# Kernel tuning notes

Measured on AMD Instinct MI355X. Metric: run time of the kernel, lower is better.

## Reference

```python
import jax, jax.numpy as jnp
import numpy as np

N = 50000
D = 128
E = 600000
ALPHA = 0.1
THETA = 0.5
LAYER = 1


def setup_inputs() -> dict:
    key = jax.random.key(0)
    k1, k2, k3, k4, k5, k6 = jax.random.split(key, 6)
    x = jax.random.normal(k1, (N, D), dtype=jnp.float32)
    x0 = jax.random.normal(k2, (N, D), dtype=jnp.float32)
    edge_index = jax.random.randint(k3, (2, E), 0, N, dtype=jnp.int64)
    norm = jax.random.uniform(k4, (E,), dtype=jnp.float32)
    # Linear weight, torch nn.Linear default init: U(-1/sqrt(fan_in), 1/sqrt(fan_in))
    bound = 1.0 / np.sqrt(D)
    W = jax.random.uniform(k5, (D, D), dtype=jnp.float32, minval=-bound, maxval=bound)
    return {"x": x, "x0": x0, "edge_index": edge_index, "norm": norm, "W": W}


def reference(x, x0, edge_index, norm, W):
    row, col = edge_index[0], edge_index[1]
    # gather source features, scale per-edge, scatter-add into destinations
    msgs = x[row] * norm[:, None]                      # [E, D]
    h = jax.ops.segment_sum(msgs, col, num_segments=N)  # [N, D]
    h = (1.0 - ALPHA) * h + ALPHA * x0
    beta = np.log(THETA / LAYER + 1.0).astype(np.float32)
    # lin(h) = h @ W.T (torch Linear applies x @ W^T)
    h = (1.0 - beta) * h + beta * (h @ W.T)
    return h
```

## Files before the change

### kernel.cpp

```cpp
#include <hip/hip_runtime.h>

#define DIM 128
#define ALPHA 0.1f
#define BETA 0.40546510810816438f

typedef __attribute__((ext_vector_type(8))) short short8v;
typedef __attribute__((ext_vector_type(4))) float float4v;

static __device__ inline unsigned short f2bf(float f) {
  union { float f; unsigned u; } a;
  a.f = f;
  unsigned r = a.u + 0x7fff + ((a.u >> 16) & 1);
  return (unsigned short)(r >> 16);
}

__global__ __launch_bounds__(256) void prep(const int* __restrict__ col,
                                            int* __restrict__ counts,
                                            int* __restrict__ rank,
                                            const float* __restrict__ x,
                                            short* __restrict__ xb,
                                            const float* __restrict__ W,
                                            short* __restrict__ Wb,
                                            int E, int total4, int cntBlocks,
                                            int cvtXBlocks) {
  int b = blockIdx.x;
  if (b < cntBlocks) {
    int e = b * 256 + threadIdx.x;
    if (e < E) rank[e] = atomicAdd(&counts[col[e]], 1);
  } else if (b < cntBlocks + cvtXBlocks) {
    int i = (b - cntBlocks) * 256 + threadIdx.x;
    if (i < total4) {
      float4 v = ((const float4*)x)[i];
      ((short4*)xb)[i] = make_short4((short)f2bf(v.x), (short)f2bf(v.y),
                                     (short)f2bf(v.z), (short)f2bf(v.w));
    }
  } else {
    int i = (b - cntBlocks - cvtXBlocks) * 256 + threadIdx.x;
    if (i < 128 * 32) {
      float4 v = ((const float4*)W)[i];
      ((short4*)Wb)[i] = make_short4((short)f2bf(v.x), (short)f2bf(v.y),
                                     (short)f2bf(v.z), (short)f2bf(v.w));
    }
  }
}

__global__ __launch_bounds__(256) void scan_blocks(const int* __restrict__ counts,
                                                   int* __restrict__ offsets,
                                                   int* __restrict__ blockSums, int N) {
  __shared__ int sm[256];
  int tid = threadIdx.x;
  int gid = blockIdx.x * 256 + tid;
  int v = (gid < N) ? counts[gid] : 0;
  sm[tid] = v;
  __syncthreads();
  for (int off = 1; off < 256; off <<= 1) {
    int t = (tid >= off) ? sm[tid - off] : 0;
    __syncthreads();
    sm[tid] += t;
    __syncthreads();
  }
  if (gid < N) offsets[gid] = sm[tid] - v;
  if (tid == 255) blockSums[blockIdx.x] = sm[255];
}

__global__ __launch_bounds__(256) void scan_off(int* __restrict__ offsets,
                                                const int* __restrict__ blockSums,
                                                int N, int E, int nb) {
  __shared__ int sm[256];
  int tid = threadIdx.x;
  int v = (tid < nb) ? blockSums[tid] : 0;
  sm[tid] = v;
  __syncthreads();
  for (int off = 1; off < 256; off <<= 1) {
    int t = (tid >= off) ? sm[tid - off] : 0;
    __syncthreads();
    sm[tid] += t;
    __syncthreads();
  }
  int excl = sm[tid] - v;
  __syncthreads();
  sm[tid] = excl;
  __syncthreads();
  int pref = sm[blockIdx.x];

  int gid = blockIdx.x * 256 + tid;
  if (gid < N) offsets[gid] += pref;
  else if (gid == N) offsets[N] = E;
}

__global__ __launch_bounds__(256) void fill_edges(const int* __restrict__ row,
                                                  const int* __restrict__ col,
                                                  const float* __restrict__ nrm,
                                                  const int* __restrict__ offsets,
                                                  const int* __restrict__ rank,
                                                  int2* __restrict__ emeta, int E) {
  int e = blockIdx.x * 256 + threadIdx.x;
  if (e >= E) return;
  int c = col[e];
  int idx = offsets[c] + rank[e];
  float s = (1.0f - ALPHA) * nrm[e];
  emeta[idx] = make_int2(row[e], __float_as_int(s));
}

__global__ __launch_bounds__(256) void gather_gemm(const unsigned* __restrict__ xb,
                                                   const float* __restrict__ x0,
                                                   const int* __restrict__ offs,
                                                   const int2* __restrict__ emeta,
                                                   const short* __restrict__ Wb,
                                                   float* __restrict__ out, int N) {
  __shared__ unsigned short hb[16][136];
  const int tid = threadIdx.x;
  const int lane = tid & 63;
  const int wave = tid >> 6;
  const int row0 = blockIdx.x * 16;

  for (int q = 0; q < 4; ++q) {
    const int lr = wave * 4 + q;
    const int n = row0 + lr;
    unsigned packed = 0;
    if (n < N) {
      int s = offs[n], t = offs[n + 1];
      float accx[8], accy[8];
#pragma unroll
      for (int j = 0; j < 8; ++j) { accx[j] = 0.0f; accy[j] = 0.0f; }
      for (int base = s; base < t; base += 64) {
        int r = 0;
        float sc = 0.0f;
        if (base + lane < t) {
          int2 m = emeta[base + lane];
          r = m.x;
          sc = __int_as_float(m.y);
        }
        int cnt = t - base;
        if (cnt > 64) cnt = 64;
        int cnt8 = (cnt + 7) & ~7;
        for (int i = 0; i < cnt8; i += 8) {
#pragma unroll
          for (int j = 0; j < 8; ++j) {
            int rj = __shfl(r, i + j);
            float sj = __shfl(sc, i + j);
            unsigned u = xb[(size_t)rj * (DIM / 2) + lane];
            accx[j] += sj * __uint_as_float(u << 16);
            accy[j] += sj * __uint_as_float(u & 0xffff0000u);
          }
        }
      }
      float sx = ((accx[0] + accx[1]) + (accx[2] + accx[3])) +
                 ((accx[4] + accx[5]) + (accx[6] + accx[7]));
      float sy = ((accy[0] + accy[1]) + (accy[2] + accy[3])) +
                 ((accy[4] + accy[5]) + (accy[6] + accy[7]));
      float2 v0 = *(const float2*)(x0 + (size_t)n * DIM + 2 * lane);
      float hx = sx + ALPHA * v0.x;
      float hy = sy + ALPHA * v0.y;
      packed = (unsigned)f2bf(hx) | ((unsigned)f2bf(hy) << 16);
    }
    *(unsigned*)&hb[lr][2 * lane] = packed;
  }
  __syncthreads();

  const int arow = lane & 15;
  const int kg = (lane >> 4) * 8;
  short8v a[4];
#pragma unroll
  for (int s = 0; s < 4; ++s) a[s] = *(const short8v*)&hb[arow][s * 32 + kg];

#pragma unroll
  for (int j2 = 0; j2 < 2; ++j2) {
    const int jt = wave * 2 + j2;
    const int bcol = jt * 16 + (lane & 15);
    float4v acc = {0.0f, 0.0f, 0.0f, 0.0f};
#pragma unroll
    for (int s = 0; s < 4; ++s) {
      short8v b = *(const short8v*)(Wb + (size_t)bcol * DIM + s * 32 + kg);
      acc = __builtin_amdgcn_mfma_f32_16x16x32_bf16(a[s], b, acc, 0, 0, 0);
    }
    const int lr0 = (lane >> 4) << 2;
#pragma unroll
    for (int p = 0; p < 4; ++p) {
      int R = row0 + lr0 + p;
      if (R < N) {
        int c = jt * 16 + (lane & 15);
        float hv = __uint_as_float(((unsigned)hb[lr0 + p][c]) << 16);
        out[(size_t)R * DIM + c] = (1.0f - BETA) * hv + BETA * acc[p];
      }
    }
  }
}

__global__ __launch_bounds__(256) void count_edges(const int* __restrict__ col,
                                                   int* __restrict__ counts,
                                                   int* __restrict__ rank, int E) {
  int e = blockIdx.x * 256 + threadIdx.x;
  if (e < E) rank[e] = atomicAdd(&counts[col[e]], 1);
}

__global__ __launch_bounds__(256) void gather_nodes_f32(const float* __restrict__ x,
                                                        const float* __restrict__ x0,
                                                        const int* __restrict__ offs,
                                                        const int2* __restrict__ emeta,
                                                        float* __restrict__ h, int N) {
  int lane = threadIdx.x & 63;
  int gwave = blockIdx.x * 4 + (threadIdx.x >> 6);
  int nwaves = gridDim.x * 4;
  int dbase = 2 * lane;
  for (int n = gwave; n < N; n += nwaves) {
    int s = offs[n], t = offs[n + 1];
    float ax = 0, ay = 0, bx = 0, by = 0;
    for (int base = s; base < t; base += 64) {
      int r = 0;
      float sc = 0.0f;
      if (base + lane < t) {
        int2 m = emeta[base + lane];
        r = m.x;
        sc = __int_as_float(m.y);
      }
      int cnt = t - base;
      if (cnt > 64) cnt = 64;
      int cnt4 = (cnt + 3) & ~3;
      for (int i = 0; i < cnt4; i += 4) {
        int r0 = __shfl(r, i), r1 = __shfl(r, i + 1);
        int r2 = __shfl(r, i + 2), r3 = __shfl(r, i + 3);
        float s0 = __shfl(sc, i), s1 = __shfl(sc, i + 1);
        float s2 = __shfl(sc, i + 2), s3 = __shfl(sc, i + 3);
        float2 v0 = *(const float2*)(x + (size_t)r0 * DIM + dbase);
        float2 v1 = *(const float2*)(x + (size_t)r1 * DIM + dbase);
        float2 v2 = *(const float2*)(x + (size_t)r2 * DIM + dbase);
        float2 v3 = *(const float2*)(x + (size_t)r3 * DIM + dbase);
        ax += s0 * v0.x; ay += s0 * v0.y;
        bx += s1 * v1.x; by += s1 * v1.y;
        ax += s2 * v2.x; ay += s2 * v2.y;
        bx += s3 * v3.x; by += s3 * v3.y;
      }
    }
    float2 v0 = *(const float2*)(x0 + (size_t)n * DIM + dbase);
    float2 hv;
    hv.x = (ax + bx) + ALPHA * v0.x;
    hv.y = (ay + by) + ALPHA * v0.y;
    *(float2*)(h + (size_t)n * DIM + dbase) = hv;
  }
}

__global__ __launch_bounds__(256) void final_mfma(const float* __restrict__ W,
                                                  float* __restrict__ out, int N) {
  __shared__ short W_s[128][136];
  __shared__ short h_s[64][136];
  const int tid = threadIdx.x;
  const int lane = tid & 63;
  const int wave = tid >> 6;
  const int row0 = blockIdx.x * 64;

  for (int idx = tid; idx < 128 * 32; idx += 256) {
    int r = idx >> 5, c4 = idx & 31;
    float4 v = ((const float4*)(W + (size_t)r * DIM))[c4];
    *(short4*)&W_s[r][c4 * 4] = make_short4((short)f2bf(v.x), (short)f2bf(v.y),
                                            (short)f2bf(v.z), (short)f2bf(v.w));
  }
  for (int idx = tid; idx < 64 * 32; idx += 256) {
    int r = idx >> 5, c4 = idx & 31;
    int R = row0 + r;
    short4 sv = make_short4(0, 0, 0, 0);
    if (R < N) {
      float4 v = ((const float4*)(out + (size_t)R * DIM))[c4];
      sv = make_short4((short)f2bf(v.x), (short)f2bf(v.y), (short)f2bf(v.z),
                       (short)f2bf(v.w));
    }
    *(short4*)&h_s[r][c4 * 4] = sv;
  }
  __syncthreads();

  const int wr0 = wave * 16;
  const int arow = wr0 + (lane & 15);
  const int kg = (lane >> 4) * 8;
  short8v a[4];
#pragma unroll
  for (int s = 0; s < 4; ++s) a[s] = *(const short8v*)&h_s[arow][s * 32 + kg];

#pragma unroll
  for (int jt = 0; jt < 8; ++jt) {
    const int bcol = jt * 16 + (lane & 15);
    float4v acc = {0.0f, 0.0f, 0.0f, 0.0f};
#pragma unroll
    for (int s = 0; s < 4; ++s) {
      short8v b = *(const short8v*)&W_s[bcol][s * 32 + kg];
      acc = __builtin_amdgcn_mfma_f32_16x16x32_bf16(a[s], b, acc, 0, 0, 0);
    }
    const int rbase = row0 + wr0 + ((lane >> 4) << 2);
#pragma unroll
    for (int p = 0; p < 4; ++p) {
      int R = rbase + p;
      if (R < N) {
        size_t off = (size_t)R * DIM + jt * 16 + (lane & 15);
        out[off] = (1.0f - BETA) * out[off] + BETA * acc[p];
      }
    }
  }
}

__global__ __launch_bounds__(256) void init_h(const float* __restrict__ x0,
                                              float* __restrict__ h, int total4) {
  int i = blockIdx.x * 256 + threadIdx.x;
  if (i < total4) {
    float4 v = ((const float4*)x0)[i];
    v.x *= ALPHA; v.y *= ALPHA; v.z *= ALPHA; v.w *= ALPHA;
    ((float4*)h)[i] = v;
  }
}

__global__ __launch_bounds__(256) void scatter_edges(const float* __restrict__ x,
                                                     const int* __restrict__ row,
                                                     const int* __restrict__ col,
                                                     const float* __restrict__ nrm,
                                                     float* __restrict__ h, int E) {
  int gid = blockIdx.x * 256 + threadIdx.x;
  int e = gid >> 5;
  if (e >= E) return;
  int d4 = (gid & 31) << 2;
  int r = row[e];
  int c = col[e];
  float s = (1.0f - ALPHA) * nrm[e];
  const float4 v = *(const float4*)(x + (size_t)r * DIM + d4);
  float* dst = h + (size_t)c * DIM + d4;
  atomicAdd(dst + 0, s * v.x);
  atomicAdd(dst + 1, s * v.y);
  atomicAdd(dst + 2, s * v.z);
  atomicAdd(dst + 3, s * v.w);
}

extern "C" void kernel_launch(void* const* d_in, const int* in_sizes, int n_in,
                              void* d_out, int out_size, void* d_ws, size_t ws_size,
                              hipStream_t stream) {
  const float* x = (const float*)d_in[0];
  const float* x0 = (const float*)d_in[1];
  const int* ei = (const int*)d_in[2];
  const float* nrm = (const float*)d_in[3];
  const float* W = (const float*)d_in[4];
  float* out = (float*)d_out;

  const int N = in_sizes[0] / DIM;
  const int E = in_sizes[2] / 2;
  const int* row = ei;
  const int* col = ei + E;

  const size_t csrNeed =
      (size_t)(2 * (N + 1) + 256 + E) * sizeof(int) + (size_t)E * 8;
  const size_t fullNeed =
      csrNeed + (size_t)N * DIM * sizeof(short) + 128 * 128 * sizeof(short);

  const int eBlocks = (E + 255) / 256;
  const int nBlocks = (N + 255) / 256;
  const int n1Blocks = (N + 256) / 256;

  if (ws_size >= csrNeed && nBlocks <= 256) {
    int* counts = (int*)d_ws;
    int* offsets = counts + (N + 1);
    int* blockSums = offsets + (N + 1);
    int* rank = blockSums + 256;
    int2* emeta = (int2*)(rank + E);
    short* xb = (short*)(emeta + E);
    short* Wb = xb + (size_t)N * DIM;

    hipMemsetAsync(counts, 0, (size_t)(N + 1) * sizeof(int), stream);

    if (ws_size >= fullNeed) {
      const int total4 = N * DIM / 4;
      const int cvtXBlocks = (total4 + 255) / 256;
      const int prepBlocks = eBlocks + cvtXBlocks + 16;
      hipLaunchKernelGGL(prep, dim3(prepBlocks), dim3(256), 0, stream, col, counts, rank, x, xb,
                         W, Wb, E, total4, eBlocks, cvtXBlocks);
      hipLaunchKernelGGL(scan_blocks, dim3(nBlocks), dim3(256), 0, stream, counts, offsets,
                         blockSums, N);
      hipLaunchKernelGGL(scan_off, dim3(n1Blocks), dim3(256), 0, stream, offsets, blockSums, N, E,
                         nBlocks);
      hipLaunchKernelGGL(fill_edges, dim3(eBlocks), dim3(256), 0, stream, row, col, nrm, offsets,
                         rank, emeta, E);
      const int t16 = (N + 15) / 16;
      hipLaunchKernelGGL(gather_gemm, dim3(t16), dim3(256), 0, stream, (const unsigned*)xb, x0,
                         offsets, emeta, Wb, out, N);
    } else {
      hipLaunchKernelGGL(count_edges, dim3(eBlocks), dim3(256), 0, stream, col, counts, rank, E);
      hipLaunchKernelGGL(scan_blocks, dim3(nBlocks), dim3(256), 0, stream, counts, offsets,
                         blockSums, N);
      hipLaunchKernelGGL(scan_off, dim3(n1Blocks), dim3(256), 0, stream, offsets, blockSums, N, E,
                         nBlocks);
      hipLaunchKernelGGL(fill_edges, dim3(eBlocks), dim3(256), 0, stream, row, col, nrm, offsets,
                         rank, emeta, E);
      const int gBlocks = (N + 3) / 4;
      hipLaunchKernelGGL(gather_nodes_f32, dim3(gBlocks), dim3(256), 0, stream, x, x0, offsets,
                         emeta, out, N);
      hipLaunchKernelGGL(final_mfma, dim3((N + 63) / 64), dim3(256), 0, stream, W, out, N);
    }
  } else {
    int total4 = N * DIM / 4;
    hipLaunchKernelGGL(init_h, dim3((total4 + 255) / 256), dim3(256), 0, stream, x0, out, total4);
    long long threads = (long long)E * 32;
    hipLaunchKernelGGL(scatter_edges, dim3((int)((threads + 255) / 256)), dim3(256), 0, stream, x,
                       row, col, nrm, out, E);
    hipLaunchKernelGGL(final_mfma, dim3((N + 63) / 64), dim3(256), 0, stream, W, out, N);
  }
}
```

Before: 102.4 us.

## Fuse two-pass offset scan into single-pass chained scan; prefetch edge metadata in gather

After: 339.7 us. 232% more time.

```diff
diff --git a/kernel.cpp b/kernel.cpp
--- a/kernel.cpp
+++ b/kernel.cpp
@@ -44,12 +44,16 @@
   }
 }
 
-__global__ __launch_bounds__(256) void scan_blocks(const int* __restrict__ counts,
-                                                   int* __restrict__ offsets,
-                                                   int* __restrict__ blockSums, int N) {
+__global__ __launch_bounds__(256) void scan_fused(const int* __restrict__ counts,
+                                                  int* __restrict__ offsets,
+                                                  int* __restrict__ flags,
+                                                  int* __restrict__ totals,
+                                                  int N, int E) {
   __shared__ int sm[256];
-  int tid = threadIdx.x;
-  int gid = blockIdx.x * 256 + tid;
+  __shared__ int smP;
+  const int tid = threadIdx.x;
+  const int b = blockIdx.x;
+  const int gid = b * 256 + tid;
   int v = (gid < N) ? counts[gid] : 0;
   sm[tid] = v;
   __syncthreads();
@@ -59,32 +63,22 @@
     sm[tid] += t;
     __syncthreads();
   }
-  if (gid < N) offsets[gid] = sm[tid] - v;
-  if (tid == 255) blockSums[blockIdx.x] = sm[255];
-}
-
-__global__ __launch_bounds__(256) void scan_off(int* __restrict__ offsets,
-                                                const int* __restrict__ blockSums,
-                                                int N, int E, int nb) {
-  __shared__ int sm[256];
-  int tid = threadIdx.x;
-  int v = (tid < nb) ? blockSums[tid] : 0;
-  sm[tid] = v;
+  int incl = sm[tid];
+  int T = sm[255];
+  if (tid == 0) {
+    int P = 0;
+    if (b > 0) {
+      while (atomicAdd(&flags[b - 1], 0) == 0) {}
+      P = atomicAdd(&totals[b - 1], 0);
+    }
+    smP = P;
+    atomicExch(&totals[b], P + T);
+    __threadfence();
+    atomicExch(&flags[b], 1);
+  }
   __syncthreads();
-  for (int off = 1; off < 256; off <<= 1) {
-    int t = (tid >= off) ? sm[tid - off] : 0;
-    __syncthreads();
-    sm[tid] += t;
-    __syncthreads();
-  }
-  int excl = sm[tid] - v;
-  __syncthreads();
-  sm[tid] = excl;
-  __syncthreads();
-  int pref = sm[blockIdx.x];
-
-  int gid = blockIdx.x * 256 + tid;
-  if (gid < N) offsets[gid] += pref;
+  int P = smP;
+  if (gid < N) offsets[gid] = P + incl - v;
   else if (gid == N) offsets[N] = E;
 }
 
@@ -114,25 +108,38 @@
   const int wave = tid >> 6;
   const int row0 = blockIdx.x * 16;
 
+  const int basen = row0 + wave * 4;
+  int o[5];
+#pragma unroll
+  for (int k = 0; k < 5; ++k) {
+    int nn = basen + k;
+    o[k] = offs[nn <= N ? nn : N];
+  }
+
+  int2 mcur = make_int2(0, 0);
+  if (o[0] + lane < o[1]) mcur = emeta[o[0] + lane];
+
+#pragma unroll
   for (int q = 0; q < 4; ++q) {
+    const int ss = o[q], tt = o[q + 1];
+    int2 mnext = make_int2(0, 0);
+    if (q < 3 && o[q + 1] + lane < o[q + 2]) mnext = emeta[o[q + 1] + lane];
+
     const int lr = wave * 4 + q;
     const int n = row0 + lr;
     unsigned packed = 0;
     if (n < N) {
-      int s = offs[n], t = offs[n + 1];
+      float2 v0 = *(const float2*)(x0 + (size_t)n * DIM + 2 * lane);
       float accx[8], accy[8];
 #pragma unroll
       for (int j = 0; j < 8; ++j) { accx[j] = 0.0f; accy[j] = 0.0f; }
-      for (int base = s; base < t; base += 64) {
-        int r = 0;
-        float sc = 0.0f;
-        if (base + lane < t) {
-          int2 m = emeta[base + lane];
-          r = m.x;
-          sc = __int_as_float(m.y);
-        }
-        int cnt = t - base;
+
+      {
+        int r = mcur.x;
+        float sc = __int_as_float(mcur.y);
+        int cnt = tt - ss;
         if (cnt > 64) cnt = 64;
+        if (cnt < 0) cnt = 0;
         int cnt8 = (cnt + 7) & ~7;
         for (int i = 0; i < cnt8; i += 8) {
 #pragma unroll
@@ -145,16 +152,38 @@
           }
         }
       }
+      for (int base = ss + 64; base < tt; base += 64) {
+        int r = 0;
+        float sc = 0.0f;
+        if (base + lane < tt) {
+          int2 m = emeta[base + lane];
+          r = m.x;
+          sc = __int_as_float(m.y);
+        }
+        int cnt = tt - base;
+        if (cnt > 64) cnt = 64;
+        int cnt8 = (cnt + 7) & ~7;
+        for (int i = 0; i < cnt8; i += 8) {
+#pragma unroll
+          for (int j = 0; j < 8; ++j) {
+            int rj = __shfl(r, i + j);
+            float sj = __shfl(sc, i + j);
+            unsigned u = xb[(size_t)rj * (DIM / 2) + lane];
+            accx[j] += sj * __uint_as_float(u << 16);
+            accy[j] += sj * __uint_as_float(u & 0xffff0000u);
+          }
+        }
+      }
       float sx = ((accx[0] + accx[1]) + (accx[2] + accx[3])) +
                  ((accx[4] + accx[5]) + (accx[6] + accx[7]));
       float sy = ((accy[0] + accy[1]) + (accy[2] + accy[3])) +
                  ((accy[4] + accy[5]) + (accy[6] + accy[7]));
-      float2 v0 = *(const float2*)(x0 + (size_t)n * DIM + 2 * lane);
       float hx = sx + ALPHA * v0.x;
       float hy = sy + ALPHA * v0.y;
       packed = (unsigned)f2bf(hx) | ((unsigned)f2bf(hy) << 16);
     }
     *(unsigned*)&hb[lr][2 * lane] = packed;
+    mcur = mnext;
   }
   __syncthreads();
 
@@ -342,24 +371,24 @@
   const int* col = ei + E;
 
   const size_t csrNeed =
-      (size_t)(2 * (N + 1) + 256 + E) * sizeof(int) + (size_t)E * 8;
+      (size_t)(2 * (N + 1) + 512 + E) * sizeof(int) + (size_t)E * 8;
   const size_t fullNeed =
       csrNeed + (size_t)N * DIM * sizeof(short) + 128 * 128 * sizeof(short);
 
   const int eBlocks = (E + 255) / 256;
   const int nBlocks = (N + 255) / 256;
-  const int n1Blocks = (N + 256) / 256;
 
   if (ws_size >= csrNeed && nBlocks <= 256) {
     int* counts = (int*)d_ws;
-    int* offsets = counts + (N + 1);
-    int* blockSums = offsets + (N + 1);
-    int* rank = blockSums + 256;
+    int* flags = counts + (N + 1);
+    int* offsets = flags + 256;
+    int* totals = offsets + (N + 1);
+    int* rank = totals + 256;
     int2* emeta = (int2*)(rank + E);
     short* xb = (short*)(emeta + E);
     short* Wb = xb + (size_t)N * DIM;
 
-    hipMemsetAsync(counts, 0, (size_t)(N + 1) * sizeof(int), stream);
+    hipMemsetAsync(counts, 0, (size_t)(N + 1 + 256) * sizeof(int), stream);
 
     if (ws_size >= fullNeed) {
       const int total4 = N * DIM / 4;
@@ -367,10 +396,8 @@
       const int prepBlocks = eBlocks + cvtXBlocks + 16;
       hipLaunchKernelGGL(prep, dim3(prepBlocks), dim3(256), 0, stream, col, counts, rank, x, xb,
                          W, Wb, E, total4, eBlocks, cvtXBlocks);
-      hipLaunchKernelGGL(scan_blocks, dim3(nBlocks), dim3(256), 0, stream, counts, offsets,
-                         blockSums, N);
-      hipLaunchKernelGGL(scan_off, dim3(n1Blocks), dim3(256), 0, stream, offsets, blockSums, N, E,
-                         nBlocks);
+      hipLaunchKernelGGL(scan_fused, dim3(nBlocks), dim3(256), 0, stream, counts, offsets, flags,
+                         totals, N, E);
       hipLaunchKernelGGL(fill_edges, dim3(eBlocks), dim3(256), 0, stream, row, col, nrm, offsets,
                          rank, emeta, E);
       const int t16 = (N + 15) / 16;
@@ -378,10 +405,8 @@
                          offsets, emeta, Wb, out, N);
     } else {
       hipLaunchKernelGGL(count_edges, dim3(eBlocks), dim3(256), 0, stream, col, counts, rank, E);
-      hipLaunchKernelGGL(scan_blocks, dim3(nBlocks), dim3(256), 0, stream, counts, offsets,
-                         blockSums, N);
-      hipLaunchKernelGGL(scan_off, dim3(n1Blocks), dim3(256), 0, stream, offsets, blockSums, N, E,
-                         nBlocks);
+      hipLaunchKernelGGL(scan_fused, dim3(nBlocks), dim3(256), 0, stream, counts, offsets, flags,
+                         totals, N, E);
       hipLaunchKernelGGL(fill_edges, dim3(eBlocks), dim3(256), 0, stream, row, col, nrm, offsets,
                          rank, emeta, E);
       const int gBlocks = (N + 3) / 4;
```
